# Kernel tuning notes

Hardware: AMD Instinct MI355X
Metric: run time of the kernel (lower is better)

The kernel has to match this reference:

```python
import jax, jax.numpy as jnp
import numpy as np

EPS = 1e-5

def _conv1x1(x, w, b):
    # x: [B,C,H,W], w: [O,C], b: [O]
    return jnp.einsum('bchw,oc->bohw', x, w) + b[None, :, None, None]

def setup_inputs() -> dict:
    key = jax.random.key(0)
    ks = jax.random.split(key, 6)
    B, C, H, W = 8, 512, 64, 64
    Ck, Cv, Co = 256, 256, 512
    x = jax.random.normal(ks[0], (B, C, H, W), dtype=jnp.float32)
    Wk = jax.random.normal(ks[1], (Ck, C), dtype=jnp.float32) * 0.02
    bk = jnp.zeros((Ck,), dtype=jnp.float32)
    gamma = jnp.ones((Ck,), dtype=jnp.float32)
    beta = jnp.zeros((Ck,), dtype=jnp.float32)
    Wv = jax.random.normal(ks[2], (Cv, C), dtype=jnp.float32) * 0.02
    bv = jnp.zeros((Cv,), dtype=jnp.float32)
    Ww = jax.random.normal(ks[3], (Co, Cv), dtype=jnp.float32) * 0.02
    bw = jnp.zeros((Co,), dtype=jnp.float32)
    return {'x': x, 'Wk': Wk, 'bk': bk, 'gamma': gamma, 'beta': beta,
            'Wv': Wv, 'bv': bv, 'Ww': Ww, 'bw': bw}

def reference(x, Wk, bk, gamma, beta, Wv, bv, Ww, bw):
    B, C, H, W = x.shape
    # f_key == f_query (shared module): conv1x1 -> BN (training stats) -> ReLU
    qk = _conv1x1(x, Wk, bk)                      # [B,Ck,H,W]
    mean = qk.mean(axis=(0, 2, 3))
    var = qk.var(axis=(0, 2, 3))                  # biased variance, as torch BN training
    feat = jax.nn.relu((qk - mean[None, :, None, None])
                       * jax.lax.rsqrt(var + EPS)[None, :, None, None]
                       * gamma[None, :, None, None] + beta[None, :, None, None])
    value = _conv1x1(x, Wv, bv)                   # [B,Cv,H,W]
    Ck = feat.shape[1]
    Cv = value.shape[1]
    N = H * W
    q = feat.reshape(B, Ck, N).transpose(0, 2, 1)  # [B,N,Ck]
    k = feat.reshape(B, Ck, N)                     # [B,Ck,N]
    v = value.reshape(B, Cv, N).transpose(0, 2, 1) # [B,N,Cv]
    scale = Ck ** (-0.5)
    sim = jax.nn.softmax(jnp.matmul(q, k) * scale, axis=-1)  # [B,N,N]
    ctx = jnp.matmul(sim, v)                       # [B,N,Cv]
    ctx = ctx.transpose(0, 2, 1).reshape(B, Cv, H, W)
    out = _conv1x1(ctx, Ww, bw)                    # [B,Co,H,W]
    # scale==1 -> visualize_* upsamples are identity; sim_map visual is None
    return (out, feat, feat, value)
```

## Files before the change

kernel.cpp:

```cpp
#include <hip/hip_runtime.h>
#include <math.h>

constexpr int  Bn  = 8;
constexpr int  Cin = 512;
constexpr int  Nn  = 4096;
constexpr int  Ck  = 256;
constexpr int  Cv  = 256;
constexpr int  Co  = 512;

constexpr size_t F1_OFF  = (size_t)Bn * Co * Nn;
constexpr size_t F2_OFF  = F1_OFF + (size_t)Bn * Ck * Nn;
constexpr size_t VAL_OFF = F2_OFF + (size_t)Bn * Ck * Nn;

typedef __attribute__((ext_vector_type(8)))  short  short8;
typedef __attribute__((ext_vector_type(16))) float  f32x16;
typedef __attribute__((ext_vector_type(8)))  ushort ushort8;

static __device__ __forceinline__ ushort f2bf(float f) {
    union { float f; unsigned u; } x; x.f = f;
    unsigned r = x.u + 0x7fffu + ((x.u >> 16) & 1u);
    return (ushort)(r >> 16);
}

__global__ __launch_bounds__(256) void cast_w(const float* __restrict__ a,
                                              const float* __restrict__ b,
                                              const float* __restrict__ c,
                                              ushort* __restrict__ da,
                                              ushort* __restrict__ db,
                                              ushort* __restrict__ dc)
{
    const int tid   = blockIdx.x * 256 + threadIdx.x;
    const int which = tid >> 14;
    const int off   = (tid & 16383) * 8;
    const float* s = (which == 0) ? a : (which == 1) ? b : c;
    ushort*      d = (which == 0) ? da : (which == 1) ? db : dc;
    const float4 u = *(const float4*)(s + off);
    const float4 v = *(const float4*)(s + off + 4);
    ushort8 o;
    o[0] = f2bf(u.x); o[1] = f2bf(u.y); o[2] = f2bf(u.z); o[3] = f2bf(u.w);
    o[4] = f2bf(v.x); o[5] = f2bf(v.y); o[6] = f2bf(v.z); o[7] = f2bf(v.w);
    *(ushort8*)(d + off) = o;
}

__global__ __launch_bounds__(256) void transpose_c(const float* __restrict__ src,
                                                   ushort* __restrict__ dst, int C)
{
    const int b  = blockIdx.z;
    const int c0 = blockIdx.y * 64;
    const int n0 = blockIdx.x * 64;
    const int t  = threadIdx.x;
    __shared__ float T[64][65];
#pragma unroll
    for (int p = 0; p < 16; ++p) {
        const int flat = p * 256 + t;
        const int cc = flat >> 6, nn = flat & 63;
        T[cc][nn] = src[((size_t)b * C + c0 + cc) * Nn + n0 + nn];
    }
    __syncthreads();
#pragma unroll
    for (int p = 0; p < 16; ++p) {
        const int flat = p * 256 + t;
        const int nn = flat >> 6, cc = flat & 63;
        dst[((size_t)b * Nn + n0 + nn) * C + c0 + cc] = f2bf(T[cc][nn]);
    }
}

template <int K, bool DUAL>
__global__ __launch_bounds__(256) void gemm_bf(const ushort* __restrict__ XT,
                                               const ushort* __restrict__ Wb,
                                               const float*  __restrict__ bias,
                                               float* __restrict__ out,
                                               ushort* __restrict__ out_bf,
                                               int M)
{
    const int b  = blockIdx.z;
    const int m0 = blockIdx.y * 128;
    const int n0 = blockIdx.x * 128;
    const int t  = threadIdx.x;
    const int w  = t >> 6, L = t & 63;
    const int l31 = L & 31, hl = L >> 5;
    const int wm = (w >> 1) * 64, wn = (w & 1) * 64;

    __shared__ __align__(16) short As[128][72];
    __shared__ __align__(16) short Bs[128][72];

    const ushort* Xb = XT + (size_t)b * Nn * K;

    f32x16 acc[2][2];
#pragma unroll
    for (int a = 0; a < 2; ++a)
#pragma unroll
        for (int bb = 0; bb < 2; ++bb)
#pragma unroll
            for (int r = 0; r < 16; ++r) acc[a][bb][r] = 0.f;

    for (int k0 = 0; k0 < K; k0 += 64) {
        __syncthreads();
#pragma unroll
        for (int p = 0; p < 4; ++p) {
            const int e   = p * 256 + t;
            const int row = e >> 3, ko = (e & 7) * 8;
            *(short8*)&As[row][ko] =
                *(const short8*)(Wb + (size_t)(m0 + row) * K + k0 + ko);
            *(short8*)&Bs[row][ko] =
                *(const short8*)(Xb + (size_t)(n0 + row) * K + k0 + ko);
        }
        __syncthreads();
#pragma unroll
        for (int kc = 0; kc < 4; ++kc) {
            short8 Af[2], Bf[2];
#pragma unroll
            for (int a = 0; a < 2; ++a)
                Af[a] = *(const short8*)&As[wm + a * 32 + l31][kc * 16 + hl * 8];
#pragma unroll
            for (int bb = 0; bb < 2; ++bb)
                Bf[bb] = *(const short8*)&Bs[wn + bb * 32 + l31][kc * 16 + hl * 8];
#pragma unroll
            for (int a = 0; a < 2; ++a)
#pragma unroll
                for (int bb = 0; bb < 2; ++bb)
                    acc[a][bb] = __builtin_amdgcn_mfma_f32_32x32x16_bf16(
                        Af[a], Bf[bb], acc[a][bb], 0, 0, 0);
        }
    }

#pragma unroll
    for (int a = 0; a < 2; ++a)
#pragma unroll
        for (int r = 0; r < 16; ++r) {
            const int row = (r & 3) + 8 * (r >> 2) + 4 * hl;
            const int o   = m0 + wm + a * 32 + row;
            const float bv = bias[o];
            const size_t base = ((size_t)b * M + o) * Nn + n0 + wn + l31;
#pragma unroll
            for (int bb = 0; bb < 2; ++bb) {
                const float vv = acc[a][bb][r] + bv;
                out[base + bb * 32] = vv;
                if (DUAL) out_bf[base + bb * 32] = f2bf(vv);
            }
        }
}

__global__ __launch_bounds__(256) void bn_stats(const float* __restrict__ qk,
                                                const float* __restrict__ gamma,
                                                const float* __restrict__ beta,
                                                float* __restrict__ ss)
{
    const int o = blockIdx.x;
    const int t = threadIdx.x;
    float s = 0.f, sq = 0.f;
    for (int b = 0; b < Bn; ++b) {
        const float* p = qk + ((size_t)b * Ck + o) * Nn;
        for (int n = t * 4; n < Nn; n += 1024) {
            const float4 v = *(const float4*)(p + n);
            s  += v.x + v.y + v.z + v.w;
            sq += v.x * v.x + v.y * v.y + v.z * v.z + v.w * v.w;
        }
    }
    __shared__ float rs[256], rq[256];
    rs[t] = s; rq[t] = sq;
    __syncthreads();
    for (int off = 128; off > 0; off >>= 1) {
        if (t < off) { rs[t] += rs[t + off]; rq[t] += rq[t + off]; }
        __syncthreads();
    }
    if (t == 0) {
        const float cnt  = (float)(Bn * Nn);
        const float mean = rs[0] / cnt;
        const float var  = rq[0] / cnt - mean * mean;
        const float inv  = rsqrtf(var + 1e-5f);
        const float sc   = gamma[o] * inv;
        ss[o]       = sc;
        ss[256 + o] = beta[o] - mean * sc;
    }
}

__global__ __launch_bounds__(256) void bn_relu(const float* __restrict__ qk,
                                               const float* __restrict__ ss,
                                               float* __restrict__ f1,
                                               float* __restrict__ f2)
{
    const size_t tid = (size_t)blockIdx.x * 256 + threadIdx.x;
    const size_t idx = tid * 4;
    const int o = (int)((idx >> 12) & 255);
    const float sc = ss[o], sh = ss[256 + o];
    const float4 v = *(const float4*)(qk + idx);
    float4 r;
    r.x = fmaxf(v.x * sc + sh, 0.f);
    r.y = fmaxf(v.y * sc + sh, 0.f);
    r.z = fmaxf(v.z * sc + sh, 0.f);
    r.w = fmaxf(v.w * sc + sh, 0.f);
    *(float4*)(f1 + idx) = r;
    *(float4*)(f2 + idx) = r;
}

constexpr int LDS_K_OFF = 0;
constexpr int LDS_V_OFF = 2 * 64 * 264;
constexpr int LDS_P_OFF = LDS_V_OFF + 2 * 256 * 72;
constexpr int LDS_SHORTS = LDS_P_OFF + 128 * 72;

__global__ __launch_bounds__(512, 2) void attn_mfma(const ushort* __restrict__ featT,
                                                    const ushort* __restrict__ valB,
                                                    ushort* __restrict__ ctx)
{
    extern __shared__ __align__(16) short lds[];
    auto Ks = (short (*)[64][264])(lds + LDS_K_OFF);
    auto Vs = (short (*)[256][72])(lds + LDS_V_OFF);
    auto Ps = (short (*)[72])     (lds + LDS_P_OFF);

    const int b   = blockIdx.x;
    const int i0  = blockIdx.y * 128;
    const int t   = threadIdx.x;
    const int w   = t >> 6;
    const int L   = t & 63;
    const int l31 = L & 31, hl = L >> 5;
    const int ig   = w >> 1;
    const int ch   = w & 1;
    const int row0 = ig * 32;
    const int jsel = ch * 32;
    const int cvb  = ch * 128;

    const ushort* F = featT + (size_t)b * Nn * Ck;
    const ushort* V = valB  + (size_t)b * Cv * Nn;

    short8 Qf[16];
    {
        const ushort* qp = F + ((size_t)(i0 + row0 + l31)) * Ck + hl * 8;
#pragma unroll
        for (int kc = 0; kc < 16; ++kc)
            Qf[kc] = *(const short8*)(qp + kc * 16);
    }

    f32x16 Oacc[4];
    f32x16 lacc;
#pragma unroll
    for (int r = 0; r < 16; ++r) {
        lacc[r] = 0.f;
#pragma unroll
        for (int c = 0; c < 4; ++c) Oacc[c][r] = 0.f;
    }

    short8 ones8;
#pragma unroll
    for (int i = 0; i < 8; ++i) ones8[i] = (short)0x3f80;

    constexpr float CEXP = 0.09016844005556021f;
    constexpr int NT = Nn / 64;

    short8 Kreg[4], Vreg[4];
#pragma unroll
    for (int p = 0; p < 4; ++p) {
        const int c8 = p * 512 + t;
        Kreg[p] = *(const short8*)(F + (size_t)(c8 >> 5) * Ck + (c8 & 31) * 8);
        Vreg[p] = *(const short8*)(V + (size_t)(c8 >> 3) * Nn + (c8 & 7) * 8);
    }
#pragma unroll
    for (int p = 0; p < 4; ++p) {
        const int c8 = p * 512 + t;
        *(short8*)&Ks[0][c8 >> 5][(c8 & 31) * 8] = Kreg[p];
        *(short8*)&Vs[0][c8 >> 3][(c8 & 7) * 8]  = Vreg[p];
    }
#pragma unroll
    for (int p = 0; p < 4; ++p) {
        const int c8 = p * 512 + t;
        Kreg[p] = *(const short8*)(F + (size_t)(64 + (c8 >> 5)) * Ck + (c8 & 31) * 8);
        Vreg[p] = *(const short8*)(V + (size_t)(c8 >> 3) * Nn + 64 + (c8 & 7) * 8);
    }
    __syncthreads();

    int cur = 0;
    for (int jt = 0; jt < NT; ++jt) {
        if (jt + 1 < NT) {
#pragma unroll
            for (int p = 0; p < 4; ++p) {
                const int c8 = p * 512 + t;
                *(short8*)&Ks[cur ^ 1][c8 >> 5][(c8 & 31) * 8] = Kreg[p];
                *(short8*)&Vs[cur ^ 1][c8 >> 3][(c8 & 7) * 8]  = Vreg[p];
            }
        }
        if (jt + 2 < NT) {
            const size_t j2 = (size_t)(jt + 2) * 64;
#pragma unroll
            for (int p = 0; p < 4; ++p) {
                const int c8 = p * 512 + t;
                Kreg[p] = *(const short8*)(F + (j2 + (c8 >> 5)) * Ck + (c8 & 31) * 8);
                Vreg[p] = *(const short8*)(V + (size_t)(c8 >> 3) * Nn + j2 + (c8 & 7) * 8);
            }
        }
        f32x16 S;
#pragma unroll
        for (int r = 0; r < 16; ++r) S[r] = 0.f;
#pragma unroll
        for (int kc = 0; kc < 16; ++kc) {
            const short8 Kf = *(const short8*)&Ks[cur][jsel + l31][kc * 16 + hl * 8];
            S = __builtin_amdgcn_mfma_f32_32x32x16_bf16(Qf[kc], Kf, S, 0, 0, 0);
        }
#pragma unroll
        for (int r = 0; r < 16; ++r) {
            const float p = exp2f(S[r] * CEXP);
            const int row = row0 + (r & 3) + 8 * (r >> 2) + 4 * hl;
            Ps[row][jsel + l31] = (short)f2bf(p);
        }
        __syncthreads();

#pragma unroll
        for (int kj = 0; kj < 4; ++kj) {
            const short8 Pf = *(const short8*)&Ps[row0 + l31][kj * 16 + hl * 8];
            lacc = __builtin_amdgcn_mfma_f32_32x32x16_bf16(Pf, ones8, lacc, 0, 0, 0);
#pragma unroll
            for (int cvt = 0; cvt < 4; ++cvt) {
                const short8 Vf =
                    *(const short8*)&Vs[cur][cvb + cvt * 32 + l31][kj * 16 + hl * 8];
                Oacc[cvt] =
                    __builtin_amdgcn_mfma_f32_32x32x16_bf16(Pf, Vf, Oacc[cvt], 0, 0, 0);
            }
        }
        __syncthreads();
        cur ^= 1;
    }

    ushort* C = ctx + ((size_t)b * Nn + i0 + row0) * Cv + cvb;
#pragma unroll
    for (int r = 0; r < 16; ++r) {
        const float linv = 1.0f / lacc[r];
        const int row = (r & 3) + 8 * (r >> 2) + 4 * hl;
        ushort* cp = C + (size_t)row * Cv + l31;
#pragma unroll
        for (int cvt = 0; cvt < 4; ++cvt)
            cp[cvt * 32] = f2bf(Oacc[cvt][r] * linv);
    }
}

extern "C" void kernel_launch(void* const* d_in, const int* in_sizes, int n_in,
                              void* d_out, int out_size, void* d_ws, size_t ws_size,
                              hipStream_t stream)
{
    const float* x     = (const float*)d_in[0];
    const float* Wk    = (const float*)d_in[1];
    const float* bk    = (const float*)d_in[2];
    const float* gamma = (const float*)d_in[3];
    const float* beta  = (const float*)d_in[4];
    const float* Wv    = (const float*)d_in[5];
    const float* bv    = (const float*)d_in[6];
    const float* Ww    = (const float*)d_in[7];
    const float* bw    = (const float*)d_in[8];

    float* out = (float*)d_out;
    float* f1  = out + F1_OFF;
    float* f2  = out + F2_OFF;
    float* val = out + VAL_OFF;

    ushort* xT    = (ushort*)d_ws;
    ushort* featT = xT;
    ushort* ctxb  = xT + (size_t)8388608;
    ushort* valB  = xT + (size_t)16777216;
    ushort* Wkb   = valB + (size_t)8388608;
    ushort* Wvb   = Wkb + 131072;
    ushort* Wwb   = Wvb + 131072;
    float*  ss    = (float*)(Wwb + 131072);

    static bool attn_attr_set = false;
    if (!attn_attr_set) {
        (void)hipFuncSetAttribute((const void*)attn_mfma,
                                  hipFuncAttributeMaxDynamicSharedMemorySize,
                                  LDS_SHORTS * 2);
        attn_attr_set = true;
    }

    cast_w<<<192, 256, 0, stream>>>(Wk, Wv, Ww, Wkb, Wvb, Wwb);
    transpose_c<<<dim3(Nn / 64, Cin / 64, Bn), 256, 0, stream>>>(x, xT, Cin);
    gemm_bf<512, false><<<dim3(Nn / 128, Ck / 128, Bn), 256, 0, stream>>>(
        xT, Wkb, bk, f1, nullptr, Ck);
    gemm_bf<512, true><<<dim3(Nn / 128, Cv / 128, Bn), 256, 0, stream>>>(
        xT, Wvb, bv, val, valB, Cv);
    bn_stats<<<Ck, 256, 0, stream>>>(f1, gamma, beta, ss);
    bn_relu<<<(Bn * Ck * Nn) / (256 * 4), 256, 0, stream>>>(f1, ss, f1, f2);
    transpose_c<<<dim3(Nn / 64, Ck / 64, Bn), 256, 0, stream>>>(f1, featT, Ck);
    attn_mfma<<<dim3(Bn, Nn / 128), 512, LDS_SHORTS * 2, stream>>>(featT, valB, ctxb);
    gemm_bf<256, false><<<dim3(Nn / 128, Co / 128, Bn), 256, 0, stream>>>(
        ctxb, Wwb, bw, out, nullptr, Co);
}
```

Measured before the change: 477.8 us.

## Restructure attention with async global-to-LDS loads, register-resident P and split-K waves

The attention kernel now stages K and V tiles directly from global memory into swizzled LDS with global_load_lds, replacing the register staging path. Each wave pair now splits the 64-key tile so that each wave computes S for its own half. The probabilities are repacked in registers with permlane32_swap rather than written to and read back from an LDS P buffer. The row sum is accumulated in scalar registers instead of through a ones-vector MFMA. Partial outputs from the two waves are reduced through LDS at the end, and s_setprio is placed around the MFMA blocks. The aim is to remove LDS round trips, bank conflicts and one barrier per tile, at the cost of a larger accumulator register footprint and hand-written waitcnt synchronisation.

```diff
diff --git a/kernel.cpp b/kernel.cpp
--- a/kernel.cpp
+++ b/kernel.cpp
@@ -20,6 +20,12 @@
     union { float f; unsigned u; } x; x.f = f;
     unsigned r = x.u + 0x7fffu + ((x.u >> 16) & 1u);
     return (ushort)(r >> 16);
+}
+
+static __device__ __forceinline__ void gll16(const void* g, void* l) {
+    __builtin_amdgcn_global_load_lds(
+        (const __attribute__((address_space(1))) void*)g,
+        (__attribute__((address_space(3))) void*)l, 16, 0, 0);
 }
 
 __global__ __launch_bounds__(256) void cast_w(const float* __restrict__ a,
@@ -194,19 +200,15 @@
     *(float4*)(f2 + idx) = r;
 }
 
-constexpr int LDS_K_OFF = 0;
-constexpr int LDS_V_OFF = 2 * 64 * 264;
-constexpr int LDS_P_OFF = LDS_V_OFF + 2 * 256 * 72;
-constexpr int LDS_SHORTS = LDS_P_OFF + 128 * 72;
+constexpr int LDS_BYTES = 132096;
 
 __global__ __launch_bounds__(512, 2) void attn_mfma(const ushort* __restrict__ featT,
                                                     const ushort* __restrict__ valB,
                                                     ushort* __restrict__ ctx)
 {
-    extern __shared__ __align__(16) short lds[];
-    auto Ks = (short (*)[64][264])(lds + LDS_K_OFF);
-    auto Vs = (short (*)[256][72])(lds + LDS_V_OFF);
-    auto Ps = (short (*)[72])     (lds + LDS_P_OFF);
+    extern __shared__ __align__(16) char lds[];
+    char* ldsK = lds;
+    char* ldsV = lds + 65536;
 
     const int b   = blockIdx.x;
     const int i0  = blockIdx.y * 128;
@@ -214,120 +216,179 @@
     const int w   = t >> 6;
     const int L   = t & 63;
     const int l31 = L & 31, hl = L >> 5;
-    const int ig   = w >> 1;
-    const int ch   = w & 1;
-    const int row0 = ig * 32;
+    const int ig  = w >> 1;
+    const int ch  = w & 1;
     const int jsel = ch * 32;
-    const int cvb  = ch * 128;
+    const int swzl = l31 << 4;
+    const int swzv = (l31 & 7) << 4;
 
     const ushort* F = featT + (size_t)b * Nn * Ck;
     const ushort* V = valB  + (size_t)b * Cv * Nn;
+    const char*   Vg = (const char*)V;
+
+    constexpr float CEXP = 0.09016844005556021f;
+    constexpr int NT = Nn / 64;
+
+#define STAGE(J0, BUF) do {                                                    \
+        const char* Kg_ = (const char*)(F + (size_t)(J0) * Ck);                \
+        char* Kd_ = ldsK + (BUF) * 32768;                                      \
+        char* Vd_ = ldsV + (BUF) * 32768;                                      \
+        _Pragma("unroll")                                                      \
+        for (int p_ = 0; p_ < 4; ++p_) {                                       \
+            const int c_ = w * 4 + p_;                                         \
+            const int o_ = c_ * 1024 + L * 16;                                 \
+            const int sK_ = ((o_ >> 9) & 31) << 4;                             \
+            gll16(Kg_ + (o_ ^ sK_), Kd_ + c_ * 1024);                          \
+            const int rV_ = o_ >> 7;                                           \
+            const int sV_ = (rV_ & 7) << 4;                                    \
+            gll16(Vg + (size_t)rV_ * (Nn * 2) + (size_t)(J0) * 2               \
+                     + ((o_ & 127) ^ sV_), Vd_ + c_ * 1024);                   \
+        }                                                                      \
+    } while (0)
+
+    STAGE(0, 0);
 
     short8 Qf[16];
     {
-        const ushort* qp = F + ((size_t)(i0 + row0 + l31)) * Ck + hl * 8;
+        const ushort* qp = F + ((size_t)(i0 + ig * 32 + l31)) * Ck + hl * 8;
 #pragma unroll
         for (int kc = 0; kc < 16; ++kc)
             Qf[kc] = *(const short8*)(qp + kc * 16);
     }
 
-    f32x16 Oacc[4];
-    f32x16 lacc;
-#pragma unroll
-    for (int r = 0; r < 16; ++r) {
-        lacc[r] = 0.f;
-#pragma unroll
-        for (int c = 0; c < 4; ++c) Oacc[c][r] = 0.f;
-    }
-
-    short8 ones8;
-#pragma unroll
-    for (int i = 0; i < 8; ++i) ones8[i] = (short)0x3f80;
-
-    constexpr float CEXP = 0.09016844005556021f;
-    constexpr int NT = Nn / 64;
-
-    short8 Kreg[4], Vreg[4];
-#pragma unroll
-    for (int p = 0; p < 4; ++p) {
-        const int c8 = p * 512 + t;
-        Kreg[p] = *(const short8*)(F + (size_t)(c8 >> 5) * Ck + (c8 & 31) * 8);
-        Vreg[p] = *(const short8*)(V + (size_t)(c8 >> 3) * Nn + (c8 & 7) * 8);
-    }
-#pragma unroll
-    for (int p = 0; p < 4; ++p) {
-        const int c8 = p * 512 + t;
-        *(short8*)&Ks[0][c8 >> 5][(c8 & 31) * 8] = Kreg[p];
-        *(short8*)&Vs[0][c8 >> 3][(c8 & 7) * 8]  = Vreg[p];
-    }
-#pragma unroll
-    for (int p = 0; p < 4; ++p) {
-        const int c8 = p * 512 + t;
-        Kreg[p] = *(const short8*)(F + (size_t)(64 + (c8 >> 5)) * Ck + (c8 & 31) * 8);
-        Vreg[p] = *(const short8*)(V + (size_t)(c8 >> 3) * Nn + 64 + (c8 & 7) * 8);
-    }
-    __syncthreads();
+    STAGE(64, 1);
+
+    f32x16 Oacc[8];
+#pragma unroll
+    for (int c = 0; c < 8; ++c)
+#pragma unroll
+        for (int r = 0; r < 16; ++r) Oacc[c][r] = 0.f;
+    float lsum = 0.f;
 
     int cur = 0;
     for (int jt = 0; jt < NT; ++jt) {
-        if (jt + 1 < NT) {
-#pragma unroll
-            for (int p = 0; p < 4; ++p) {
-                const int c8 = p * 512 + t;
-                *(short8*)&Ks[cur ^ 1][c8 >> 5][(c8 & 31) * 8] = Kreg[p];
-                *(short8*)&Vs[cur ^ 1][c8 >> 3][(c8 & 7) * 8]  = Vreg[p];
-            }
-        }
-        if (jt + 2 < NT) {
-            const size_t j2 = (size_t)(jt + 2) * 64;
-#pragma unroll
-            for (int p = 0; p < 4; ++p) {
-                const int c8 = p * 512 + t;
-                Kreg[p] = *(const short8*)(F + (j2 + (c8 >> 5)) * Ck + (c8 & 31) * 8);
-                Vreg[p] = *(const short8*)(V + (size_t)(c8 >> 3) * Nn + j2 + (c8 & 7) * 8);
-            }
-        }
-        f32x16 S;
-#pragma unroll
-        for (int r = 0; r < 16; ++r) S[r] = 0.f;
-#pragma unroll
-        for (int kc = 0; kc < 16; ++kc) {
-            const short8 Kf = *(const short8*)&Ks[cur][jsel + l31][kc * 16 + hl * 8];
-            S = __builtin_amdgcn_mfma_f32_32x32x16_bf16(Qf[kc], Kf, S, 0, 0, 0);
-        }
+        if (jt < NT - 1) { asm volatile("s_waitcnt vmcnt(8)" ::: "memory"); }
+        else             { asm volatile("s_waitcnt vmcnt(0)" ::: "memory"); }
+        __builtin_amdgcn_s_barrier();
+
+        const char* Kc = ldsK + cur * 32768 + (jsel + l31) * 512;
+        const char* Vc = ldsV + cur * 32768;
+
+        f32x16 Sa, Sb;
+#pragma unroll
+        for (int r = 0; r < 16; ++r) { Sa[r] = 0.f; Sb[r] = 0.f; }
+        __builtin_amdgcn_s_setprio(1);
+#pragma unroll
+        for (int kc = 0; kc < 8; ++kc) {
+            const short8 K0 = *(const short8*)(Kc + ((kc * 64      + hl * 16) ^ swzl));
+            const short8 K1 = *(const short8*)(Kc + ((kc * 64 + 32 + hl * 16) ^ swzl));
+            Sa = __builtin_amdgcn_mfma_f32_32x32x16_bf16(K0, Qf[2 * kc],     Sa, 0, 0, 0);
+            Sb = __builtin_amdgcn_mfma_f32_32x32x16_bf16(K1, Qf[2 * kc + 1], Sb, 0, 0, 0);
+        }
+        __builtin_amdgcn_s_setprio(0);
+
+        unsigned pb[16];
 #pragma unroll
         for (int r = 0; r < 16; ++r) {
-            const float p = exp2f(S[r] * CEXP);
-            const int row = row0 + (r & 3) + 8 * (r >> 2) + 4 * hl;
-            Ps[row][jsel + l31] = (short)f2bf(p);
-        }
-        __syncthreads();
-
-#pragma unroll
-        for (int kj = 0; kj < 4; ++kj) {
-            const short8 Pf = *(const short8*)&Ps[row0 + l31][kj * 16 + hl * 8];
-            lacc = __builtin_amdgcn_mfma_f32_32x32x16_bf16(Pf, ones8, lacc, 0, 0, 0);
-#pragma unroll
-            for (int cvt = 0; cvt < 4; ++cvt) {
-                const short8 Vf =
-                    *(const short8*)&Vs[cur][cvb + cvt * 32 + l31][kj * 16 + hl * 8];
-                Oacc[cvt] =
-                    __builtin_amdgcn_mfma_f32_32x32x16_bf16(Pf, Vf, Oacc[cvt], 0, 0, 0);
-            }
-        }
-        __syncthreads();
+            const float p = exp2f((Sa[r] + Sb[r]) * CEXP);
+            const unsigned ub = (unsigned)f2bf(p);
+            pb[r] = ub;
+            lsum += __uint_as_float(ub << 16);
+        }
+        short8 Pf[2];
+#pragma unroll
+        for (int g = 0; g < 2; ++g) {
+            unsigned w0 = pb[8 * g + 0] | (pb[8 * g + 1] << 16);
+            unsigned w1 = pb[8 * g + 2] | (pb[8 * g + 3] << 16);
+            unsigned w2 = pb[8 * g + 4] | (pb[8 * g + 5] << 16);
+            unsigned w3 = pb[8 * g + 6] | (pb[8 * g + 7] << 16);
+            auto s02 = __builtin_amdgcn_permlane32_swap(w0, w2, false, false);
+            auto s13 = __builtin_amdgcn_permlane32_swap(w1, w3, false, false);
+            union { unsigned u[4]; short8 s; } pu;
+            pu.u[0] = s02[0]; pu.u[1] = s13[0]; pu.u[2] = s02[1]; pu.u[3] = s13[1];
+            Pf[g] = pu.s;
+        }
+
+        __builtin_amdgcn_s_setprio(1);
+#pragma unroll
+        for (int g = 0; g < 2; ++g)
+#pragma unroll
+            for (int cvt = 0; cvt < 8; ++cvt) {
+                const short8 Vf = *(const short8*)(Vc + (cvt * 32 + l31) * 128
+                                     + ((ch * 64 + g * 32 + hl * 16) ^ swzv));
+                Oacc[cvt] = __builtin_amdgcn_mfma_f32_32x32x16_bf16(
+                    Pf[g], Vf, Oacc[cvt], 0, 0, 0);
+            }
+        __builtin_amdgcn_s_setprio(0);
+
+        asm volatile("s_waitcnt lgkmcnt(0)" ::: "memory");
+        __builtin_amdgcn_s_barrier();
+        if (jt + 2 < NT) { STAGE((size_t)(jt + 2) * 64, cur); }
         cur ^= 1;
     }
-
-    ushort* C = ctx + ((size_t)b * Nn + i0 + row0) * Cv + cvb;
-#pragma unroll
-    for (int r = 0; r < 16; ++r) {
-        const float linv = 1.0f / lacc[r];
-        const int row = (r & 3) + 8 * (r >> 2) + 4 * hl;
-        ushort* cp = C + (size_t)row * Cv + l31;
-#pragma unroll
-        for (int cvt = 0; cvt < 4; ++cvt)
-            cp[cvt * 32] = f2bf(Oacc[cvt][r] * linv);
+#undef STAGE
+
+    {
+        unsigned a = __float_as_uint(lsum), bcopy = a;
+        auto sw = __builtin_amdgcn_permlane32_swap(a, bcopy, false, false);
+        lsum = __uint_as_float(sw[0]) + __uint_as_float(sw[1]);
+    }
+    float* Lr  = (float*)(lds + 131072);
+    float* Oex = (float*)lds;
+    Lr[(ig * 2 + ch) * 32 + l31] = lsum;
+    {
+        const int dbase = (ig * 2 + ch) * 32;
+        if (ch == 0) {
+#pragma unroll
+            for (int r = 0; r < 16; ++r) {
+                const int row = (r & 3) + 8 * (r >> 2) + 4 * hl;
+#pragma unroll
+                for (int c4 = 0; c4 < 4; ++c4)
+                    Oex[(size_t)(dbase + row) * 128 + c4 * 32 + l31] = Oacc[4 + c4][r];
+            }
+        } else {
+#pragma unroll
+            for (int r = 0; r < 16; ++r) {
+                const int row = (r & 3) + 8 * (r >> 2) + 4 * hl;
+#pragma unroll
+                for (int c4 = 0; c4 < 4; ++c4)
+                    Oex[(size_t)(dbase + row) * 128 + c4 * 32 + l31] = Oacc[c4][r];
+            }
+        }
+    }
+    asm volatile("s_waitcnt lgkmcnt(0)" ::: "memory");
+    __builtin_amdgcn_s_barrier();
+
+    ushort* Cb = ctx + ((size_t)b * Nn + i0 + ig * 32) * Cv + ch * 128;
+    const int pbase = (ig * 2 + (ch ^ 1)) * 32;
+    if (ch == 0) {
+#pragma unroll
+        for (int r = 0; r < 16; ++r) {
+            const int row = (r & 3) + 8 * (r >> 2) + 4 * hl;
+            const float lt = Lr[(ig * 2) * 32 + row] + Lr[(ig * 2 + 1) * 32 + row];
+            const float linv = 1.f / lt;
+            ushort* cp = Cb + (size_t)row * Cv + l31;
+#pragma unroll
+            for (int c4 = 0; c4 < 4; ++c4) {
+                const float v = Oacc[c4][r]
+                    + Oex[(size_t)(pbase + row) * 128 + c4 * 32 + l31];
+                cp[c4 * 32] = f2bf(v * linv);
+            }
+        }
+    } else {
+#pragma unroll
+        for (int r = 0; r < 16; ++r) {
+            const int row = (r & 3) + 8 * (r >> 2) + 4 * hl;
+            const float lt = Lr[(ig * 2) * 32 + row] + Lr[(ig * 2 + 1) * 32 + row];
+            const float linv = 1.f / lt;
+            ushort* cp = Cb + (size_t)row * Cv + l31;
+#pragma unroll
+            for (int c4 = 0; c4 < 4; ++c4) {
+                const float v = Oacc[4 + c4][r]
+                    + Oex[(size_t)(pbase + row) * 128 + c4 * 32 + l31];
+                cp[c4 * 32] = f2bf(v * linv);
+            }
+        }
     }
 }
 
@@ -363,7 +424,7 @@
     if (!attn_attr_set) {
         (void)hipFuncSetAttribute((const void*)attn_mfma,
                                   hipFuncAttributeMaxDynamicSharedMemorySize,
-                                  LDS_SHORTS * 2);
+                                  LDS_BYTES);
         attn_attr_set = true;
     }
 
@@ -376,7 +437,7 @@
     bn_stats<<<Ck, 256, 0, stream>>>(f1, gamma, beta, ss);
     bn_relu<<<(Bn * Ck * Nn) / (256 * 4), 256, 0, stream>>>(f1, ss, f1, f2);
     transpose_c<<<dim3(Nn / 64, Ck / 64, Bn), 256, 0, stream>>>(f1, featT, Ck);
-    attn_mfma<<<dim3(Bn, Nn / 128), 512, LDS_SHORTS * 2, stream>>>(featT, valB, ctxb);
+    attn_mfma<<<dim3(Bn, Nn / 128), 512, LDS_BYTES, stream>>>(featT, valB, ctxb);
     gemm_bf<256, false><<<dim3(Nn / 128, Co / 128, Bn), 256, 0, stream>>>(
         ctxb, Wwb, bw, out, nullptr, Co);
 }
```

New measurement: 610.4 us. 1.28x slower.
